# Performance work log

Hardware: AMD Instinct MI355X
Metric: run time of the kernel (lower is better)

## Reference

```python
import jax, jax.numpy as jnp
import numpy as np

DT = 0.1  # leak rate of the FORCE rate-RNN cell


def setup_inputs() -> dict:
    key = jax.random.key(0)
    ks = jax.random.split(key, 6)
    N, IN, OUT, T = 192, 64, 192, 32
    alpha_P = 1.0
    x = jax.random.normal(ks[0], (1, T, IN), jnp.float32)
    y = jax.random.normal(ks[1], (1, T, OUT), jnp.float32)
    W_in = jax.random.normal(ks[2], (IN, N), jnp.float32) / np.sqrt(IN).astype(np.float32)
    W_rec = 1.5 * jax.random.normal(ks[3], (N, N), jnp.float32) / np.sqrt(N).astype(np.float32)
    W_out = jax.random.normal(ks[4], (N, OUT), jnp.float32) / np.sqrt(N).astype(np.float32)
    a0 = jax.random.normal(ks[5], (1, N), jnp.float32)
    # P_output = alpha_P * I  (keras.initializers.Identity(gain=alpha_P))
    P_output = alpha_P * jnp.eye(N, dtype=jnp.float32)
    # P_GG: identity_3d[:, i, i] = alpha_P -> each of the N slices is alpha_P * I
    P_GG = jnp.broadcast_to(alpha_P * jnp.eye(N, dtype=jnp.float32), (N, N, N)).copy()
    return dict(x=x, y=y, W_in=W_in, W_rec=W_rec, W_out=W_out, a0=a0,
                P_output=P_output, P_GG=P_GG)


def _step(carry, xy, W_in):
    a, P_o, W_o, P_g, W_r = carry
    x_t, y_t = xy  # (IN,), (N,)
    # leaky tanh rate-RNN cell (canonical tension FORCE layer)
    a = (1.0 - DT) * a + DT * (jnp.tanh(a) @ W_r + x_t[None, :] @ W_in)  # (1,N)
    h = jnp.tanh(a)[0]            # (N,)
    z = h @ W_o                   # (N,)
    # --- RLS / Sherman-Morrison update of P_output ---
    k = P_o @ h                   # (N,)
    c = 1.0 / (1.0 + h @ k)
    P_o = P_o - c * jnp.outer(k, h @ P_o)
    # --- output kernel update (uses UPDATED P_output, SGD lr=1) ---
    e = z - y_t                   # (N,)
    W_o = W_o - jnp.outer(P_o @ h, e)
    # --- per-neuron RLS update of P_GG (N,N,N) ---
    Ph = jnp.einsum('ijk,k->ij', P_g, h)      # (N,N)
    hPh = Ph @ h                              # (N,)
    htP = jnp.einsum('k,ikj->ij', h, P_g)     # (N,N)
    P_g = P_g - Ph[:, :, None] * htP[:, None, :] / (1.0 + hPh)[:, None, None]
    # --- recurrent kernel update (uses UPDATED P_GG) ---
    Ph2 = jnp.einsum('ijk,k->ij', P_g, h)     # (N,N)
    W_r = W_r - (Ph2 * e[None, :]).T
    return (a, P_o, W_o, P_g, W_r), z


def reference(x, y, W_in, W_rec, W_out, a0, P_output, P_GG):
    def step(carry, xy):
        return _step(carry, xy, W_in)
    carry0 = (a0, P_output, W_out, P_GG, W_rec)
    _, zs = jax.lax.scan(step, carry0, (x[0], y[0]))  # zs: (T, N)
    return zs[None, :, :]  # (1, T, N): readout sequence during FORCE training
```

## Files before the change

### kernel.cpp

```cpp
#include <hip/hip_runtime.h>
#include <math.h>

#define NN   192
#define NIN  64
#define NT   32
#define BLK  192
#define NW   3

typedef unsigned long long u64;
typedef unsigned int u32;

struct WS {
  u32 hrep [NN][NN];
  u64 ekrep[NN][NN];
};

#define REP48(M) M(0)M(1)M(2)M(3)M(4)M(5)M(6)M(7)M(8)M(9)M(10)M(11)M(12)M(13)M(14)M(15)M(16)M(17)M(18)M(19)M(20)M(21)M(22)M(23)M(24)M(25)M(26)M(27)M(28)M(29)M(30)M(31)M(32)M(33)M(34)M(35)M(36)M(37)M(38)M(39)M(40)M(41)M(42)M(43)M(44)M(45)M(46)M(47)

__device__ __forceinline__ u32 pack_h(float v, u32 tag) {
  return (__float_as_uint(v) & ~0xFFu) | tag;
}
__device__ __forceinline__ u64 pack_ek(float e, float k, u32 tag) {
  return ((u64)((__float_as_uint(e) & ~0xFFu) | tag) << 32)
       |  (u64)((__float_as_uint(k) & ~0xFFu) | tag);
}

__device__ __forceinline__ float poll_h(u32* p, u32 tag) {
  u32 v; long g = 0;
  while (true) {
    v = __hip_atomic_load(p, __ATOMIC_RELAXED, __HIP_MEMORY_SCOPE_AGENT);
    if ((v & 0xFFu) == tag) break;
    __builtin_amdgcn_s_sleep(1);
    if (++g > 30000000L) break;
  }
  return __uint_as_float(v & ~0xFFu);
}

__device__ __forceinline__ float2 poll_ek(u64* p, u32 tag) {
  u64 v; long g = 0;
  while (true) {
    v = __hip_atomic_load(p, __ATOMIC_RELAXED, __HIP_MEMORY_SCOPE_AGENT);
    if ((((u32)v & 0xFFu) == tag) & (((u32)(v >> 32) & 0xFFu) == tag)) break;
    __builtin_amdgcn_s_sleep(1);
    if (++g > 30000000L) break;
  }
  return make_float2(__uint_as_float((u32)(v >> 32) & ~0xFFu),
                     __uint_as_float((u32)v & ~0xFFu));
}

template <int K>
__device__ __forceinline__ void block_reduceK(float* v, float (*red)[NW], int w, int l) {
  #pragma unroll
  for (int o = 32; o > 0; o >>= 1) {
    #pragma unroll
    for (int q = 0; q < K; ++q) v[q] += __shfl_xor(v[q], o, 64);
  }
  if (l == 0) {
    #pragma unroll
    for (int q = 0; q < K; ++q) red[q][w] = v[q];
  }
  __syncthreads();
  #pragma unroll
  for (int q = 0; q < K; ++q) v[q] = red[q][0] + red[q][1] + red[q][2];
}

extern "C" __global__ void __launch_bounds__(BLK, 1)
force_persistent(const float* __restrict__ x,   const float* __restrict__ y,
                 const float* __restrict__ Win, const float* __restrict__ Wrec,
                 const float* __restrict__ Wout,const float* __restrict__ a0,
                 const float* __restrict__ Pout,const float* __restrict__ Pgg,
                 float* __restrict__ out, WS* __restrict__ ws)
{
  const int b   = blockIdx.x;
  const int tid = threadIdx.x;
  const int w   = tid >> 6;
  const int l   = tid & 63;

  __shared__ __align__(16) float hsS[NN];
  __shared__ __align__(16) float phS[NN];
  __shared__ float red5[2][5][NW];
  __shared__ float red3[2][3][NW];
  __shared__ float xwS[NT];
  __shared__ float yS [NT];

  if (w == 0) {
    const float wv = Win[l * NN + b];
    float c[NT];
    #pragma unroll
    for (int t2 = 0; t2 < NT; ++t2) c[t2] = x[t2 * NIN + l] * wv;
    #pragma unroll
    for (int o = 32; o > 0; o >>= 1) {
      #pragma unroll
      for (int t2 = 0; t2 < NT; ++t2) c[t2] += __shfl_xor(c[t2], o, 64);
    }
    if (l == 0) {
      #pragma unroll
      for (int t2 = 0; t2 < NT; ++t2) xwS[t2] = c[t2];
    }
  } else if (w == 1 && l < NT) {
    yS[l] = y[l * NN + b];
  }

  float wrt = Wrec[tid * NN + b];
  float wot = Wout[tid * NN + b];
  float po  = Pout[b * NN + tid];

  float a_run;
  {
    float v0[1] = { tanhf(a0[tid]) * wrt };
    block_reduceK<1>(v0, red3[1], w, l);
    a_run = 0.9f * a0[b] + 0.1f * (v0[0] + xwS[0]);
    __hip_atomic_store(&ws->hrep[tid][b], pack_h(tanhf(a_run), 1u),
                       __ATOMIC_RELAXED, __HIP_MEMORY_SCOPE_AGENT);
  }

  #define SDECL(r) float4 s##r;
  REP48(SDECL)
  {
    const float4* srow = (const float4*)(Pgg + (size_t)b * NN * NN + (size_t)tid * NN);
    #define SLOAD(r) s##r = srow[r];
    REP48(SLOAD)
  }

  float p_prev = 0.f, rden_prev = 0.f, c_prev = 0.f;
  float e_prev_own = 0.f, k_prev_own = 0.f, e_b_prev = 0.f, k_b_prev = 0.f;

  #pragma unroll 1
  for (int t = 0; t < NT; ++t) {
    const u32 tag = (u32)(t + 1);
    const int par = t & 1;

    const float h_own = poll_h(&ws->hrep[b][tid], tag);
    hsS[tid] = h_own;

    float v[5];
    v[0] = h_own * wrt;
    v[1] = h_own * (p_prev * e_prev_own);
    v[2] = h_own * wot;
    v[3] = h_own * k_prev_own;
    v[4] = h_own * po;
    block_reduceK<5>(v, red5[par], w, l);
    const float ssum_half = v[0] - rden_prev * v[1];
    const float g   = v[3];
    const float z   = v[2] - c_prev * e_b_prev * g;
    const float kb  = v[4] - c_prev * k_b_prev * g;
    const float eb  = z - yS[t];
    __hip_atomic_store(&ws->ekrep[tid][b], pack_ek(eb, kb, tag),
                       __ATOMIC_RELAXED, __HIP_MEMORY_SCOPE_AGENT);
    if (tid == 0) out[t * NN + b] = z;
    if (t == NT - 1) break;

    wrt -= rden_prev * p_prev * e_prev_own;
    wot -= c_prev * k_prev_own * e_b_prev;
    po  -= c_prev * k_b_prev  * k_prev_own;

    const float4* h4 = (const float4*)hsS;
    float4 acc = make_float4(0.f, 0.f, 0.f, 0.f);
    #define PHC(r) { const float4 hv = h4[r]; \
                     acc.x += s##r.x*hv.x; acc.y += s##r.y*hv.y; \
                     acc.z += s##r.z*hv.z; acc.w += s##r.w*hv.w; }
    REP48(PHC)
    const float p = (acc.x + acc.y) + (acc.z + acc.w);
    phS[tid] = p;

    const float2 ek = poll_ek(&ws->ekrep[b][tid], tag);
    const float e_own = ek.x, k_own = ek.y;

    float u[3];
    u[0] = k_own * h_own;
    u[1] = h_own * p * e_own;
    u[2] = p * h_own;
    block_reduceK<3>(u, red3[par], w, l);
    const float rden = 1.f / (1.f + u[2]);
    const float c1   = 1.f / (1.f + u[0]);

    a_run = 0.9f * a_run + 0.1f * (ssum_half - rden * u[1] + xwS[t + 1]);
    const float hnext = tanhf(a_run);
    __hip_atomic_store(&ws->hrep[tid][b], pack_h(hnext, tag + 1u),
                       __ATOMIC_RELAXED, __HIP_MEMORY_SCOPE_AGENT);

    const float rv = rden * p;
    const float4* ph4 = (const float4*)phS;
    #define PHD(r) { const float4 pv = ph4[r]; \
                     s##r.x -= rv*pv.x; s##r.y -= rv*pv.y; \
                     s##r.z -= rv*pv.z; s##r.w -= rv*pv.w; }
    REP48(PHD)

    p_prev = p; rden_prev = rden; c_prev = c1;
    e_prev_own = e_own; k_prev_own = k_own; e_b_prev = eb; k_b_prev = kb;
  }
}

extern "C" void kernel_launch(void* const* d_in, const int* in_sizes, int n_in,
                              void* d_out, int out_size, void* d_ws, size_t ws_size,
                              hipStream_t stream) {
  const float* x    = (const float*)d_in[0];
  const float* y    = (const float*)d_in[1];
  const float* Win  = (const float*)d_in[2];
  const float* Wrec = (const float*)d_in[3];
  const float* Wout = (const float*)d_in[4];
  const float* a0   = (const float*)d_in[5];
  const float* Pout = (const float*)d_in[6];
  const float* Pgg  = (const float*)d_in[7];
  float* out = (float*)d_out;
  WS* ws = (WS*)d_ws;
  (void)in_sizes; (void)n_in; (void)out_size; (void)ws_size;

  hipMemsetAsync(ws, 0, sizeof(WS), stream);
  force_persistent<<<NN, BLK, 0, stream>>>(x, y, Win, Wrec, Wout, a0, Pout, Pgg, out, ws);
}
```

Before: 151.5 us.

## Replace per-reader broadcast copies with eight shared replicas and full-precision tagged slots

Result: faster. 144.4 us (-4.7%).

```diff
diff --git a/kernel.cpp b/kernel.cpp
--- a/kernel.cpp
+++ b/kernel.cpp
@@ -6,46 +6,44 @@
 #define NT   32
 #define BLK  192
 #define NW   3
+#define NREP 8
 
 typedef unsigned long long u64;
 typedef unsigned int u32;
 
+struct HSlot { u64 v; u64 pad; };
 struct WS {
-  u32 hrep [NN][NN];
-  u64 ekrep[NN][NN];
+  HSlot hrep [NREP][NN];
+  u64   ekrep[NREP][NN][2];
 };
 
 #define REP48(M) M(0)M(1)M(2)M(3)M(4)M(5)M(6)M(7)M(8)M(9)M(10)M(11)M(12)M(13)M(14)M(15)M(16)M(17)M(18)M(19)M(20)M(21)M(22)M(23)M(24)M(25)M(26)M(27)M(28)M(29)M(30)M(31)M(32)M(33)M(34)M(35)M(36)M(37)M(38)M(39)M(40)M(41)M(42)M(43)M(44)M(45)M(46)M(47)
 
-__device__ __forceinline__ u32 pack_h(float v, u32 tag) {
-  return (__float_as_uint(v) & ~0xFFu) | tag;
-}
-__device__ __forceinline__ u64 pack_ek(float e, float k, u32 tag) {
-  return ((u64)((__float_as_uint(e) & ~0xFFu) | tag) << 32)
-       |  (u64)((__float_as_uint(k) & ~0xFFu) | tag);
-}
-
-__device__ __forceinline__ float poll_h(u32* p, u32 tag) {
-  u32 v; long g = 0;
-  while (true) {
-    v = __hip_atomic_load(p, __ATOMIC_RELAXED, __HIP_MEMORY_SCOPE_AGENT);
-    if ((v & 0xFFu) == tag) break;
-    __builtin_amdgcn_s_sleep(1);
-    if (++g > 30000000L) break;
-  }
-  return __uint_as_float(v & ~0xFFu);
-}
-
-__device__ __forceinline__ float2 poll_ek(u64* p, u32 tag) {
+__device__ __forceinline__ u64 packf(float v, u32 tag) {
+  return ((u64)tag << 32) | (u64)__float_as_uint(v);
+}
+
+__device__ __forceinline__ float poll_slot(u64* p, u32 tag) {
   u64 v; long g = 0;
   while (true) {
     v = __hip_atomic_load(p, __ATOMIC_RELAXED, __HIP_MEMORY_SCOPE_AGENT);
-    if ((((u32)v & 0xFFu) == tag) & (((u32)(v >> 32) & 0xFFu) == tag)) break;
-    __builtin_amdgcn_s_sleep(1);
+    if ((u32)(v >> 32) == tag) break;
+    __builtin_amdgcn_s_sleep(2);
     if (++g > 30000000L) break;
   }
-  return make_float2(__uint_as_float((u32)(v >> 32) & ~0xFFu),
-                     __uint_as_float((u32)v & ~0xFFu));
+  return __uint_as_float((u32)v);
+}
+
+__device__ __forceinline__ float2 poll_ek(u64* p, u32 tag) {
+  u64 va, vb; long g = 0;
+  while (true) {
+    va = __hip_atomic_load(p,     __ATOMIC_RELAXED, __HIP_MEMORY_SCOPE_AGENT);
+    vb = __hip_atomic_load(p + 1, __ATOMIC_RELAXED, __HIP_MEMORY_SCOPE_AGENT);
+    if (((u32)(va >> 32) == tag) & ((u32)(vb >> 32) == tag)) break;
+    __builtin_amdgcn_s_sleep(2);
+    if (++g > 30000000L) break;
+  }
+  return make_float2(__uint_as_float((u32)va), __uint_as_float((u32)vb));
 }
 
 template <int K>
@@ -75,6 +73,7 @@
   const int tid = threadIdx.x;
   const int w   = tid >> 6;
   const int l   = tid & 63;
+  const int rep = b & (NREP - 1);
 
   __shared__ __align__(16) float hsS[NN];
   __shared__ __align__(16) float phS[NN];
@@ -110,8 +109,10 @@
     float v0[1] = { tanhf(a0[tid]) * wrt };
     block_reduceK<1>(v0, red3[1], w, l);
     a_run = 0.9f * a0[b] + 0.1f * (v0[0] + xwS[0]);
-    __hip_atomic_store(&ws->hrep[tid][b], pack_h(tanhf(a_run), 1u),
-                       __ATOMIC_RELAXED, __HIP_MEMORY_SCOPE_AGENT);
+    const float h0 = tanhf(a_run);
+    if (tid < NREP)
+      __hip_atomic_store(&ws->hrep[tid][b].v, packf(h0, 1u),
+                         __ATOMIC_RELAXED, __HIP_MEMORY_SCOPE_AGENT);
   }
 
   #define SDECL(r) float4 s##r;
@@ -130,7 +131,7 @@
     const u32 tag = (u32)(t + 1);
     const int par = t & 1;
 
-    const float h_own = poll_h(&ws->hrep[b][tid], tag);
+    const float h_own = poll_slot(&ws->hrep[rep][tid].v, tag);
     hsS[tid] = h_own;
 
     float v[5];
@@ -145,8 +146,12 @@
     const float z   = v[2] - c_prev * e_b_prev * g;
     const float kb  = v[4] - c_prev * k_b_prev * g;
     const float eb  = z - yS[t];
-    __hip_atomic_store(&ws->ekrep[tid][b], pack_ek(eb, kb, tag),
-                       __ATOMIC_RELAXED, __HIP_MEMORY_SCOPE_AGENT);
+    if (tid < NREP) {
+      __hip_atomic_store(&ws->ekrep[tid][b][0], packf(eb, tag),
+                         __ATOMIC_RELAXED, __HIP_MEMORY_SCOPE_AGENT);
+      __hip_atomic_store(&ws->ekrep[tid][b][1], packf(kb, tag),
+                         __ATOMIC_RELAXED, __HIP_MEMORY_SCOPE_AGENT);
+    }
     if (tid == 0) out[t * NN + b] = z;
     if (t == NT - 1) break;
 
@@ -163,7 +168,7 @@
     const float p = (acc.x + acc.y) + (acc.z + acc.w);
     phS[tid] = p;
 
-    const float2 ek = poll_ek(&ws->ekrep[b][tid], tag);
+    const float2 ek = poll_ek(&ws->ekrep[rep][tid][0], tag);
     const float e_own = ek.x, k_own = ek.y;
 
     float u[3];
@@ -176,8 +181,9 @@
 
     a_run = 0.9f * a_run + 0.1f * (ssum_half - rden * u[1] + xwS[t + 1]);
     const float hnext = tanhf(a_run);
-    __hip_atomic_store(&ws->hrep[tid][b], pack_h(hnext, tag + 1u),
-                       __ATOMIC_RELAXED, __HIP_MEMORY_SCOPE_AGENT);
+    if (tid < NREP)
+      __hip_atomic_store(&ws->hrep[tid][b].v, packf(hnext, tag + 1u),
+                         __ATOMIC_RELAXED, __HIP_MEMORY_SCOPE_AGENT);
 
     const float rv = rden * p;
     const float4* ph4 = (const float4*)phS;
```
